# Optimization experiments

Measured on AMD Instinct MI355X. Metric: run time of the kernel, lower is better.

The kernel has to match this reference:

```python
import jax, jax.numpy as jnp
import numpy as np

EMBED_DIM = 1024
FFN_DIM = 4096
N_QUBITS = 10


def setup_inputs() -> dict:
    key = jax.random.key(0)
    k_x, k_phi, k_w1, k_w2 = jax.random.split(key, 4)
    x = jax.random.normal(k_x, (8, 2048, EMBED_DIM), dtype=jnp.float32)
    # trainable RY angles, one per wire (torchquantum init ~ U(0, 2pi); any init works for a reference)
    ry_params = jax.random.uniform(k_phi, (N_QUBITS,), dtype=jnp.float32, minval=0.0, maxval=2.0 * np.pi)
    # nn.Linear(n_qubits, ffn_dim, bias=False): weight [ffn_dim, n_qubits]
    w1 = jax.random.normal(k_w1, (FFN_DIM, N_QUBITS), dtype=jnp.float32) / np.sqrt(N_QUBITS)
    # nn.Linear(ffn_dim, embed_dim, bias=False): weight [embed_dim, ffn_dim]
    w2 = jax.random.normal(k_w2, (EMBED_DIM, FFN_DIM), dtype=jnp.float32) / np.sqrt(FFN_DIM)
    return {"x": x, "ry_params": ry_params, "w1": w1, "w2": w2}


def reference(x, ry_params, w1, w2):
    # Quantum layer in closed form: wires are unentangled.
    # |0> --RX(x_i)--RY(phi_i)--> <Z_i> = cos(x_i) * cos(phi_i)
    # Only the first N_QUBITS features of each token are encoded.
    q_out = jnp.cos(x[..., :N_QUBITS]) * jnp.cos(ry_params)  # [B, S, nq]
    # dropout is identity in eval mode
    h = jnp.einsum('bsq,fq->bsf', q_out, w1)  # [B, S, ffn]
    h = jax.nn.relu(h)
    return jnp.einsum('bsf,ef->bse', h, w2)  # [B, S, embed]
```

## Files before the change

kernel.cpp:

```cpp
#include <hip/hip_runtime.h>
#include <hip/hip_bf16.h>
#include <stdint.h>

#define M_TOK   16384
#define EMBED   1024
#define FFN     4096
#define NQ      10

typedef __attribute__((ext_vector_type(8))) short  bf16x8;
typedef __attribute__((ext_vector_type(4))) float  f32x4;
typedef __attribute__((ext_vector_type(8))) unsigned short u16x8;

static __device__ __forceinline__ unsigned short f2bf(float f) {
    union { float f; unsigned u; } v; v.f = f;
    unsigned r = v.u + 0x7FFF + ((v.u >> 16) & 1);
    return (unsigned short)(r >> 16);
}

__global__ __launch_bounds__(256) void compute_h(
    const float* __restrict__ x, const float* __restrict__ ry,
    const float* __restrict__ w1, unsigned short* __restrict__ h)
{
    __shared__ float cq[32 * 16];
    __shared__ float cry[NQ];

    const int tid = threadIdx.x;
    const int t0  = blockIdx.x * 32;
    const int fb  = blockIdx.y * 2048 + tid * 8;

    if (tid < NQ) cry[tid] = cosf(ry[tid]);
    for (int idx = tid; idx < 32 * NQ; idx += 256) {
        int t = idx / NQ;
        int i = idx - t * NQ;
        cq[t * 16 + i] = cosf(x[(size_t)(t0 + t) * EMBED + i]);
    }
    __syncthreads();

    float wf[8][NQ];
#pragma unroll
    for (int fi = 0; fi < 8; ++fi)
#pragma unroll
        for (int i = 0; i < NQ; ++i)
            wf[fi][i] = w1[(fb + fi) * NQ + i] * cry[i];

    for (int t = 0; t < 32; ++t) {
        const float4 c0 = *(const float4*)&cq[t * 16 + 0];
        const float4 c1 = *(const float4*)&cq[t * 16 + 4];
        const float2 c2 = *(const float2*)&cq[t * 16 + 8];
        u16x8 v;
#pragma unroll
        for (int fi = 0; fi < 8; ++fi) {
            float s = c0.x * wf[fi][0] + c0.y * wf[fi][1] + c0.z * wf[fi][2]
                    + c0.w * wf[fi][3] + c1.x * wf[fi][4] + c1.y * wf[fi][5]
                    + c1.z * wf[fi][6] + c1.w * wf[fi][7] + c2.x * wf[fi][8]
                    + c2.y * wf[fi][9];
            v[fi] = f2bf(fmaxf(s, 0.f));
        }
        *(u16x8*)(h + (size_t)(t0 + t) * FFN + fb) = v;
    }
}

__global__ __launch_bounds__(256) void conv_w2(
    const float* __restrict__ w2, unsigned short* __restrict__ o)
{
    const int idx = (blockIdx.x * 256 + threadIdx.x) * 8;
    float4 a = *(const float4*)(w2 + idx);
    float4 b = *(const float4*)(w2 + idx + 4);
    u16x8 v;
    v[0] = f2bf(a.x); v[1] = f2bf(a.y); v[2] = f2bf(a.z); v[3] = f2bf(a.w);
    v[4] = f2bf(b.x); v[5] = f2bf(b.y); v[6] = f2bf(b.z); v[7] = f2bf(b.w);
    *(u16x8*)(o + idx) = v;
}

#define GK 4096
#define GN 1024
#define BK 64

#define GL2LDS(g, l) \
    __builtin_amdgcn_global_load_lds( \
        (const __attribute__((address_space(1))) void*)(g), \
        (__attribute__((address_space(3))) void*)(l), 16, 0, 0)

__global__ __launch_bounds__(256) void gemm_bt(
    const unsigned short* __restrict__ A,
    const unsigned short* __restrict__ B,
    float* __restrict__ C)
{
    __shared__ unsigned short At[128 * BK];
    __shared__ unsigned short Bt[128 * BK];

    const int tid  = threadIdx.x;
    const int wv   = tid >> 6;
    const int lane = tid & 63;

    const int bid   = blockIdx.x;
    const int group = bid >> 6;
    const int g     = bid & 63;
    const int m_blk = group * 8 + (g & 7);
    const int n_blk = g >> 3;
    const int m0 = m_blk * 128;
    const int n0 = n_blk * 128;

    const int wr = (wv & 1) * 64;
    const int wc = (wv >> 1) * 64;

    f32x4 acc[4][4] = {};

    const int srow  = lane >> 3;
    const int scolb = ((lane & 7) ^ srow) * 16;

    const int rr = lane & 15;
    const int cc = lane >> 4;
    const int f0off = rr * 128 + (((0 * 4 + cc) ^ (rr & 7)) * 16);
    const int f1off = rr * 128 + (((1 * 4 + cc) ^ (rr & 7)) * 16);

    for (int k0 = 0; k0 < GK; k0 += BK) {
#pragma unroll
        for (int j = 0; j < 4; ++j) {
            const int rbase = wv * 32 + j * 8;
            const char* ag = (const char*)A +
                (((size_t)(m0 + rbase + srow) * GK + k0) * 2 + scolb);
            GL2LDS(ag, (char*)At + rbase * 128);
            const char* bg = (const char*)B +
                (((size_t)(n0 + rbase + srow) * GK + k0) * 2 + scolb);
            GL2LDS(bg, (char*)Bt + rbase * 128);
        }
        __syncthreads();

#pragma unroll
        for (int s = 0; s < 2; ++s) {
            const int foff = s ? f1off : f0off;
            bf16x8 af[4], bf[4];
#pragma unroll
            for (int i = 0; i < 4; ++i) {
                af[i] = *(const bf16x8*)((const char*)At + (wr + i * 16) * 128 + foff);
                bf[i] = *(const bf16x8*)((const char*)Bt + (wc + i * 16) * 128 + foff);
            }
#pragma unroll
            for (int i = 0; i < 4; ++i)
#pragma unroll
                for (int j = 0; j < 4; ++j)
                    acc[i][j] = __builtin_amdgcn_mfma_f32_16x16x32_bf16(
                        af[i], bf[j], acc[i][j], 0, 0, 0);
        }
        __syncthreads();
    }

    const int cn    = lane & 15;
    const int rbase = (lane >> 4) * 4;
#pragma unroll
    for (int i = 0; i < 4; ++i)
#pragma unroll
        for (int j = 0; j < 4; ++j)
#pragma unroll
            for (int r = 0; r < 4; ++r) {
                const int m = m0 + wr + i * 16 + rbase + r;
                const int n = n0 + wc + j * 16 + cn;
                C[(size_t)m * GN + n] = acc[i][j][r];
            }
}

extern "C" void kernel_launch(void* const* d_in, const int* in_sizes, int n_in,
                              void* d_out, int out_size, void* d_ws, size_t ws_size,
                              hipStream_t stream) {
    const float* x  = (const float*)d_in[0];
    const float* ry = (const float*)d_in[1];
    const float* w1 = (const float*)d_in[2];
    const float* w2 = (const float*)d_in[3];
    float* out = (float*)d_out;

    unsigned short* h   = (unsigned short*)d_ws;
    unsigned short* w2b = (unsigned short*)((char*)d_ws +
                           (size_t)M_TOK * FFN * sizeof(unsigned short));

    compute_h<<<dim3(512, 2), 256, 0, stream>>>(x, ry, w1, h);
    conv_w2<<<dim3((EMBED * FFN) / (256 * 8)), 256, 0, stream>>>(w2, w2b);
    gemm_bt<<<dim3(1024), 256, 0, stream>>>(h, w2b, out);
}
```

Measured before the change: 293.8 us.

## Rewrite GEMM as 256x256 tiles with 4-stage LDS pipeline and 8 waves

The bf16 GEMM now uses 512-thread blocks computing 256x256 output tiles. It uses BK=32 and a 4-deep LDS ring buffer prefetched two tiles ahead with global_load_lds, interleaving split A/B loads with MFMA phases, barriers and s_setprio. This is meant to hide global memory latency and raise MFMA utilisation, since the old single-buffered loop waited on every tile load. The compute_h kernel is also retiled to 16 tokens per block with twice as many blocks. LDS usage goes up (128KB), which limits occupancy, and there is a tail of 256 blocks across the CUs.

```diff
diff --git a/kernel.cpp b/kernel.cpp
--- a/kernel.cpp
+++ b/kernel.cpp
@@ -1,5 +1,4 @@
 #include <hip/hip_runtime.h>
-#include <hip/hip_bf16.h>
 #include <stdint.h>
 
 #define M_TOK   16384
@@ -7,6 +6,11 @@
 #define FFN     4096
 #define NQ      10
 
+#define GK 4096
+#define GN 1024
+#define BK 32
+#define NT (GK / BK)
+
 typedef __attribute__((ext_vector_type(8))) short  bf16x8;
 typedef __attribute__((ext_vector_type(4))) float  f32x4;
 typedef __attribute__((ext_vector_type(8))) unsigned short u16x8;
@@ -21,17 +25,17 @@
     const float* __restrict__ x, const float* __restrict__ ry,
     const float* __restrict__ w1, unsigned short* __restrict__ h)
 {
-    __shared__ float cq[32 * 16];
+    __shared__ float cq[16 * 16];
     __shared__ float cry[NQ];
 
     const int tid = threadIdx.x;
-    const int t0  = blockIdx.x * 32;
+    const int t0  = blockIdx.x * 16;
     const int fb  = blockIdx.y * 2048 + tid * 8;
 
     if (tid < NQ) cry[tid] = cosf(ry[tid]);
-    for (int idx = tid; idx < 32 * NQ; idx += 256) {
-        int t = idx / NQ;
-        int i = idx - t * NQ;
+    if (tid < 16 * NQ) {
+        int t = tid / NQ;
+        int i = tid - t * NQ;
         cq[t * 16 + i] = cosf(x[(size_t)(t0 + t) * EMBED + i]);
     }
     __syncthreads();
@@ -43,7 +47,7 @@
         for (int i = 0; i < NQ; ++i)
             wf[fi][i] = w1[(fb + fi) * NQ + i] * cry[i];
 
-    for (int t = 0; t < 32; ++t) {
+    for (int t = 0; t < 16; ++t) {
         const float4 c0 = *(const float4*)&cq[t * 16 + 0];
         const float4 c1 = *(const float4*)&cq[t * 16 + 4];
         const float2 c2 = *(const float2*)&cq[t * 16 + 8];
@@ -72,90 +76,109 @@
     *(u16x8*)(o + idx) = v;
 }
 
-#define GK 4096
-#define GN 1024
-#define BK 64
-
 #define GL2LDS(g, l) \
     __builtin_amdgcn_global_load_lds( \
         (const __attribute__((address_space(1))) void*)(g), \
         (__attribute__((address_space(3))) void*)(l), 16, 0, 0)
 
-__global__ __launch_bounds__(256) void gemm_bt(
+__global__ __launch_bounds__(512, 2) void gemm_bt(
     const unsigned short* __restrict__ A,
     const unsigned short* __restrict__ B,
     float* __restrict__ C)
 {
-    __shared__ unsigned short At[128 * BK];
-    __shared__ unsigned short Bt[128 * BK];
+    __shared__ __align__(16) unsigned short As[4][256 * BK];
+    __shared__ __align__(16) unsigned short Bs[4][256 * BK];
 
     const int tid  = threadIdx.x;
     const int wv   = tid >> 6;
     const int lane = tid & 63;
-
-    const int bid   = blockIdx.x;
-    const int group = bid >> 6;
-    const int g     = bid & 63;
-    const int m_blk = group * 8 + (g & 7);
-    const int n_blk = g >> 3;
-    const int m0 = m_blk * 128;
-    const int n0 = n_blk * 128;
-
-    const int wr = (wv & 1) * 64;
-    const int wc = (wv >> 1) * 64;
-
-    f32x4 acc[4][4] = {};
-
-    const int srow  = lane >> 3;
-    const int scolb = ((lane & 7) ^ srow) * 16;
-
-    const int rr = lane & 15;
-    const int cc = lane >> 4;
-    const int f0off = rr * 128 + (((0 * 4 + cc) ^ (rr & 7)) * 16);
-    const int f1off = rr * 128 + (((1 * 4 + cc) ^ (rr & 7)) * 16);
-
-    for (int k0 = 0; k0 < GK; k0 += BK) {
-#pragma unroll
-        for (int j = 0; j < 4; ++j) {
-            const int rbase = wv * 32 + j * 8;
-            const char* ag = (const char*)A +
-                (((size_t)(m0 + rbase + srow) * GK + k0) * 2 + scolb);
-            GL2LDS(ag, (char*)At + rbase * 128);
-            const char* bg = (const char*)B +
-                (((size_t)(n0 + rbase + srow) * GK + k0) * 2 + scolb);
-            GL2LDS(bg, (char*)Bt + rbase * 128);
-        }
-        __syncthreads();
-
-#pragma unroll
-        for (int s = 0; s < 2; ++s) {
-            const int foff = s ? f1off : f0off;
-            bf16x8 af[4], bf[4];
-#pragma unroll
-            for (int i = 0; i < 4; ++i) {
-                af[i] = *(const bf16x8*)((const char*)At + (wr + i * 16) * 128 + foff);
-                bf[i] = *(const bf16x8*)((const char*)Bt + (wc + i * 16) * 128 + foff);
-            }
-#pragma unroll
-            for (int i = 0; i < 4; ++i)
-#pragma unroll
-                for (int j = 0; j < 4; ++j)
-                    acc[i][j] = __builtin_amdgcn_mfma_f32_16x16x32_bf16(
-                        af[i], bf[j], acc[i][j], 0, 0, 0);
-        }
-        __syncthreads();
-    }
-
-    const int cn    = lane & 15;
-    const int rbase = (lane >> 4) * 4;
-#pragma unroll
-    for (int i = 0; i < 4; ++i)
+    const int wm   = wv >> 2;
+    const int wn   = wv & 3;
+
+    const int bid = blockIdx.x;
+    const int wg  = (bid & 7) * 32 + (bid >> 3);
+    const int m0  = (wg & 63) * 256;
+    const int n0  = (wg >> 6) * 256;
+
+    const char* ag = (const char*)A +
+        ((size_t)(m0 + wv * 32 + (lane >> 2)) * GK + (lane & 3) * 8) * 2;
+    const char* bg = (const char*)B +
+        ((size_t)(n0 + wv * 32 + (lane >> 2)) * GK + (lane & 3) * 8) * 2;
+    const int ldsb = wv * 2048;
+
+    const int arow = wm * 128 + (lane & 15);
+    const int brow = wn * 64  + (lane & 15);
+    const int kch  = (lane >> 4) * 16;
+
+    f32x4 acc[8][4] = {};
+
+#pragma unroll
+    for (int P = 0; P < 2; ++P) {
+        GL2LDS(ag + P * (BK * 2),               (char*)As[P] + ldsb);
+        GL2LDS(ag + P * (BK * 2) + 16 * GK * 2, (char*)As[P] + ldsb + 1024);
+        GL2LDS(bg + P * (BK * 2),               (char*)Bs[P] + ldsb);
+        GL2LDS(bg + P * (BK * 2) + 16 * GK * 2, (char*)Bs[P] + ldsb + 1024);
+    }
+    asm volatile("s_waitcnt vmcnt(4)" ::: "memory");
+    __builtin_amdgcn_s_barrier();
+
+#pragma unroll 1
+    for (int T = 0; T < NT; ++T) {
+        const char* At = (const char*)As[T & 3];
+        const char* Bt = (const char*)Bs[T & 3];
+        char* Ad = (char*)As[(T + 2) & 3] + ldsb;
+        char* Bd = (char*)Bs[(T + 2) & 3] + ldsb;
+        const size_t ks = (T + 2 < NT) ? (size_t)(T + 2) * (BK * 2) : 0;
+
+        bf16x8 afr[4], bfr[4];
+
 #pragma unroll
         for (int j = 0; j < 4; ++j)
+            bfr[j] = *(const bf16x8*)(Bt + (brow + j * 16) * 64 + kch);
+#pragma unroll
+        for (int i = 0; i < 4; ++i)
+            afr[i] = *(const bf16x8*)(At + (arow + i * 16) * 64 + kch);
+        GL2LDS(ag + ks,               Ad);
+        GL2LDS(ag + ks + 16 * GK * 2, Ad + 1024);
+        __builtin_amdgcn_s_barrier();
+        __builtin_amdgcn_s_setprio(1);
+#pragma unroll
+        for (int i = 0; i < 4; ++i)
+#pragma unroll
+            for (int j = 0; j < 4; ++j)
+                acc[i][j] = __builtin_amdgcn_mfma_f32_16x16x32_bf16(
+                    afr[i], bfr[j], acc[i][j], 0, 0, 0);
+        __builtin_amdgcn_s_setprio(0);
+        __builtin_amdgcn_s_barrier();
+
+#pragma unroll
+        for (int i = 0; i < 4; ++i)
+            afr[i] = *(const bf16x8*)(At + (arow + 64 + i * 16) * 64 + kch);
+        GL2LDS(bg + ks,               Bd);
+        GL2LDS(bg + ks + 16 * GK * 2, Bd + 1024);
+        __builtin_amdgcn_s_barrier();
+        __builtin_amdgcn_s_setprio(1);
+#pragma unroll
+        for (int i = 0; i < 4; ++i)
+#pragma unroll
+            for (int j = 0; j < 4; ++j)
+                acc[4 + i][j] = __builtin_amdgcn_mfma_f32_16x16x32_bf16(
+                    afr[i], bfr[j], acc[4 + i][j], 0, 0, 0);
+        __builtin_amdgcn_s_setprio(0);
+        asm volatile("s_waitcnt vmcnt(4)" ::: "memory");
+        __builtin_amdgcn_s_barrier();
+    }
+
+    const int cn = lane & 15;
+    const int rb = (lane >> 4) * 4;
+#pragma unroll
+    for (int i = 0; i < 8; ++i)
+#pragma unroll
+        for (int j = 0; j < 4; ++j)
 #pragma unroll
             for (int r = 0; r < 4; ++r) {
-                const int m = m0 + wr + i * 16 + rbase + r;
-                const int n = n0 + wc + j * 16 + cn;
+                const int m = m0 + wm * 128 + i * 16 + rb + r;
+                const int n = n0 + wn * 64  + j * 16 + cn;
                 C[(size_t)m * GN + n] = acc[i][j][r];
             }
 }
@@ -173,7 +196,7 @@
     unsigned short* w2b = (unsigned short*)((char*)d_ws +
                            (size_t)M_TOK * FFN * sizeof(unsigned short));
 
-    compute_h<<<dim3(512, 2), 256, 0, stream>>>(x, ry, w1, h);
+    compute_h<<<dim3(1024, 2), 256, 0, stream>>>(x, ry, w1, h);
     conv_w2<<<dim3((EMBED * FFN) / (256 * 8)), 256, 0, stream>>>(w2, w2b);
-    gemm_bt<<<dim3(1024), 256, 0, stream>>>(h, w2b, out);
-}
+    gemm_bt<<<dim3(256), 512, 0, stream>>>(h, w2b, out);
+}
```

New measurement: 358.3 us. +22.0%, slower.
